# Kernel tuning notes

Hardware: AMD Instinct MI355X
Metric: run time of the kernel (lower is better)

Reference implementation:

```python
import jax, jax.numpy as jnp
import numpy as np

# Canonical topology: root object with K arrays, each array has L number leaves.
# Weights are tied across paths (tie_weights_containers=tie_weights_primitives=True),
# NumberEmbedder runs in eval mode with initial buffers mean=0, sqmean=1 -> identity norm.

K, L, D = 8192, 128, 64


def setup_inputs() -> dict:
    key = jax.random.key(0)
    ks = jax.random.split(key, 16)
    s = 1.0 / np.sqrt(D)
    return {
        "x": jax.random.normal(ks[0], (K, L), dtype=jnp.float32),
        "W_num": jax.random.normal(ks[1], (D, 1), dtype=jnp.float32) * s,
        "b_num": jax.random.normal(ks[2], (D,), dtype=jnp.float32) * s,
        "W_ih": jax.random.normal(ks[3], (4 * D, 2 * D), dtype=jnp.float32) * s,
        "W_hh": jax.random.normal(ks[4], (4 * D, D), dtype=jnp.float32) * s,
        "b_ih": jax.random.normal(ks[5], (4 * D,), dtype=jnp.float32) * s,
        "b_hh": jax.random.normal(ks[6], (4 * D,), dtype=jnp.float32) * s,
        "W_aout": jax.random.normal(ks[7], (D, D), dtype=jnp.float32) * s,
        "b_aout": jax.random.normal(ks[8], (D,), dtype=jnp.float32) * s,
        "W_fh": jax.random.normal(ks[9], (D, D), dtype=jnp.float32) * s,
        "b_fh": jax.random.normal(ks[10], (D,), dtype=jnp.float32) * s,
        "W_iouh": jax.random.normal(ks[11], (3 * D, D), dtype=jnp.float32) * s,
        "b_iouh": jax.random.normal(ks[12], (3 * D,), dtype=jnp.float32) * s,
        "W_oout": jax.random.normal(ks[13], (D, D), dtype=jnp.float32) * s,
        "b_oout": jax.random.normal(ks[14], (D,), dtype=jnp.float32) * s,
    }


def _forward(x, W_num, b_num, W_ih, W_hh, b_ih, b_hh, W_aout, b_aout,
             W_fh, b_fh, W_iouh, b_iouh, W_oout, b_oout):
    d = W_hh.shape[1]
    # --- NumberEmbedder: Linear(1, d) on identity-normalized numbers; c = 0 ---
    emb = x[..., None] * W_num[:, 0] + b_num          # [K, L, d]
    xs = jnp.transpose(emb, (1, 0, 2))                # [L, K, d] time-major for scan
    # --- ArrayEmbedder: LSTMCell over children; input = cat(child_h, child_c) ---
    # child_c is identically zero, so only the first half of W_ih contributes.
    W_ih_h = W_ih[:, :d]                              # [4d, d]
    bias = b_ih + b_hh                                # [4d]

    def step(carry, x_t):
        h, c = carry
        gates = x_t @ W_ih_h.T + h @ W_hh.T + bias    # [K, 4d]
        i, f, g, o = jnp.split(gates, 4, axis=1)
        c2 = jax.nn.sigmoid(f) * c + jax.nn.sigmoid(i) * jnp.tanh(g)
        h2 = jax.nn.sigmoid(o) * jnp.tanh(c2)
        return (h2, c2), None

    h0 = jnp.zeros((x.shape[0], d), dtype=x.dtype)
    (h_arr, c_arr), _ = jax.lax.scan(step, (h0, h0), xs)
    h_hat = h_arr @ W_aout.T + b_aout                 # [K, d] array lout
    # --- ObjectEmbedder: child-sum TreeLSTM over the K array states ---
    f = h_hat @ W_fh.T + b_fh                         # [K, d]
    fc_sum = jnp.sum(jax.nn.sigmoid(f) * c_arr, axis=0, keepdims=True)  # [1, d]
    hs_bar = jnp.sum(h_hat, axis=0, keepdims=True)    # [1, d]
    iou = hs_bar @ W_iouh.T + b_iouh                  # [1, 3d]
    i, o, u = jnp.split(iou, 3, axis=1)
    c_obj = jax.nn.sigmoid(i) * jnp.tanh(u) + fc_sum
    h_obj = jax.nn.sigmoid(o) * jnp.tanh(c_obj)
    h_hat_obj = h_obj @ W_oout.T + b_oout             # [1, d] object lout
    # root forward returns cat(h, c)
    return jnp.concatenate([h_hat_obj, c_obj], axis=1)  # [1, 2d]


def reference(x, W_num, b_num, W_ih, W_hh, b_ih, b_hh, W_aout, b_aout,
              W_fh, b_fh, W_iouh, b_iouh, W_oout, b_oout):
    return _forward(x, W_num, b_num, W_ih, W_hh, b_ih, b_hh, W_aout, b_aout,
                    W_fh, b_fh, W_iouh, b_iouh, W_oout, b_oout)
```

## Files before the change

### kernel.cpp

```cpp
#include <hip/hip_runtime.h>
#include <cstddef>

#define D   64
#define L   128
#define NT  256
#define ROWS 16
#define XSS 132
#define HBS 72
#define NBLK 512
#define LOG2E 1.4426950408889634f

typedef __attribute__((ext_vector_type(8))) short short8;
typedef __attribute__((ext_vector_type(4))) float floatx4;

__device__ __forceinline__ float fast_rcp(float x) {
#if defined(__has_builtin)
#if __has_builtin(__builtin_amdgcn_rcpf)
  return __builtin_amdgcn_rcpf(x);
#else
  return 1.0f / x;
#endif
#else
  return 1.0f / x;
#endif
}
__device__ __forceinline__ float ex2(float x) {
#if defined(__has_builtin)
#if __has_builtin(__builtin_amdgcn_exp2f)
  return __builtin_amdgcn_exp2f(x);
#else
  return __builtin_exp2f(x);
#endif
#else
  return __builtin_exp2f(x);
#endif
}
__device__ __forceinline__ float sig_plain(float x) {
  return fast_rcp(1.0f + ex2(-LOG2E * x));
}
__device__ __forceinline__ float tanh2(float G) {
  return fmaf(2.0f, fast_rcp(1.0f + ex2(G)), -1.0f);
}
__device__ __forceinline__ unsigned short f2bf_rtne(float f) {
  unsigned int u = __float_as_uint(f);
  u += 0x7fffu + ((u >> 16) & 1u);
  return (unsigned short)(u >> 16);
}
__device__ __forceinline__ float bf2f(unsigned short s) {
  return __uint_as_float(((unsigned int)s) << 16);
}
__device__ __forceinline__ void pack_split(float h2, short* hi, short* lo) {
  unsigned int u = __float_as_uint(h2);
  *hi = (short)(u >> 16);
  float hif = __uint_as_float(u & 0xffff0000u);
  *lo = (short)((unsigned short)(__float_as_uint(h2 - hif) >> 16));
}

__global__ __launch_bounds__(NT, 2)
void lstm_main(const float* __restrict__ x,
               const float* __restrict__ W_num,
               const float* __restrict__ b_num,
               const float* __restrict__ W_ih,
               const float* __restrict__ W_hh,
               const float* __restrict__ b_ih,
               const float* __restrict__ b_hh,
               const float* __restrict__ W_aout,
               const float* __restrict__ b_aout,
               const float* __restrict__ W_fh,
               const float* __restrict__ b_fh,
               const float* __restrict__ W_iouh,
               const float* __restrict__ b_iouh,
               const float* __restrict__ W_oout,
               const float* __restrict__ b_oout,
               float* __restrict__ acc_out,
               float* __restrict__ out)
{
  __shared__ __align__(16) float xs[ROWS * XSS];
  __shared__ __align__(16) short hb_hi[2][ROWS * HBS];
  __shared__ __align__(16) short hb_lo[2][ROWS * HBS];
  __shared__ float sacc[2 * D];
  __shared__ float hobj[D];
  __shared__ int   is_last;

  const int tid  = threadIdx.x;
  const int w    = tid >> 6;
  const int lane = tid & 63;
  const int quad = lane >> 4;
  const int c16  = lane & 15;
  const int k0   = blockIdx.x * ROWS;
  const int dcol = w * 16 + c16;

  for (int i = tid; i < ROWS * (L / 4); i += NT) {
    int r = i >> 5, c4 = i & 31;
    float4 v = ((const float4*)(x + (size_t)(k0 + r) * L))[c4];
    float* dst = &xs[r * XSS + c4 * 4];
    dst[0] = v.x; dst[1] = v.y; dst[2] = v.z; dst[3] = v.w;
  }
  for (int i = tid; i < ROWS * HBS; i += NT) { hb_hi[0][i] = 0; hb_lo[0][i] = 0; }

  const float gscale[4] = {-LOG2E, -LOG2E, -2.0f * LOG2E, -LOG2E};

  float An[4], Bc[4];
#pragma unroll
  for (int g = 0; g < 4; ++g) {
    int j = g * 64 + dcol;
    float a = 0.0f, b = b_ih[j] + b_hh[j];
    for (int e = 0; e < D; ++e) {
      float wih = W_ih[(size_t)j * (2 * D) + e];
      a = fmaf(W_num[e], wih, a);
      b = fmaf(b_num[e], wih, b);
    }
    An[g] = a * gscale[g]; Bc[g] = b * gscale[g];
  }

  short8 Bhi[4][2], Blo[4][2];
#pragma unroll
  for (int g = 0; g < 4; ++g) {
#pragma unroll
    for (int kk = 0; kk < 2; ++kk) {
      const float* wp = W_hh + (size_t)(g * 64 + dcol) * D + kk * 32 + quad * 8;
      short8 hi8, lo8;
#pragma unroll
      for (int j = 0; j < 8; ++j) {
        float v = wp[j] * gscale[g];
        unsigned short h = f2bf_rtne(v);
        hi8[j] = (short)h;
        lo8[j] = (short)f2bf_rtne(v - bf2f(h));
      }
      Bhi[g][kk] = hi8; Blo[g][kk] = lo8;
    }
  }

  float creg[4] = {0.f, 0.f, 0.f, 0.f};
  float hreg[4] = {0.f, 0.f, 0.f, 0.f};
  __syncthreads();

  int p = 0;
  for (int t4 = 0; t4 < L; t4 += 4) {
    float4 xq[4];
#pragma unroll
    for (int r = 0; r < 4; ++r)
      xq[r] = *(const float4*)&xs[(quad * 4 + r) * XSS + t4];
#pragma unroll
    for (int u = 0; u < 4; ++u) {
      short8 ahi[2], alo[2];
#pragma unroll
      for (int kk = 0; kk < 2; ++kk) {
        int off = c16 * HBS + kk * 32 + quad * 8;
        ahi[kk] = *(const short8*)&hb_hi[p][off];
        alo[kk] = *(const short8*)&hb_lo[p][off];
      }
      float xv[4] = {xq[0][u], xq[1][u], xq[2][u], xq[3][u]};
      floatx4 acc[4];
#pragma unroll
      for (int g = 0; g < 4; ++g)
        acc[g] = (floatx4){fmaf(An[g], xv[0], Bc[g]), fmaf(An[g], xv[1], Bc[g]),
                           fmaf(An[g], xv[2], Bc[g]), fmaf(An[g], xv[3], Bc[g])};
#pragma unroll
      for (int kk = 0; kk < 2; ++kk) {
#pragma unroll
        for (int g = 0; g < 4; ++g) {
          acc[g] = __builtin_amdgcn_mfma_f32_16x16x32_bf16(ahi[kk], Bhi[g][kk], acc[g], 0, 0, 0);
          acc[g] = __builtin_amdgcn_mfma_f32_16x16x32_bf16(alo[kk], Bhi[g][kk], acc[g], 0, 0, 0);
          acc[g] = __builtin_amdgcn_mfma_f32_16x16x32_bf16(ahi[kk], Blo[g][kk], acc[g], 0, 0, 0);
        }
      }
#pragma unroll
      for (int r = 0; r < 4; ++r) {
        float Ei = ex2(acc[0][r]);
        float Ef = ex2(acc[1][r]);
        float Eg = ex2(acc[2][r]);
        float Eo = ex2(acc[3][r]);
        float pf = 1.0f + Ef, pi = 1.0f + Ei, pg = 1.0f + Eg;
        float mg = 1.0f - Eg;
        float pig = pi * pg;
        float num = fmaf(creg[r], pig, mg * pf);
        float c2  = num * fast_rcp(pf * pig);
        float Ec  = ex2(-2.0f * LOG2E * c2);
        float po = 1.0f + Eo, pc = 1.0f + Ec, mc = 1.0f - Ec;
        float h2 = mc * fast_rcp(po * pc);
        creg[r] = c2;
        hreg[r] = h2;
        short hi, lo;
        pack_split(h2, &hi, &lo);
        int row = quad * 4 + r;
        hb_hi[p ^ 1][row * HBS + dcol] = hi;
        hb_lo[p ^ 1][row * HBS + dcol] = lo;
      }
      __syncthreads();
      p ^= 1;
    }
  }

#pragma unroll
  for (int r = 0; r < 4; ++r) xs[(quad * 4 + r) * XSS + dcol] = hreg[r];
  __syncthreads();

  float hhat[4];
#pragma unroll
  for (int r = 0; r < 4; ++r) {
    float a = b_aout[dcol];
    const float4* wa = (const float4*)(W_aout + (size_t)dcol * D);
    const float* hp = &xs[(quad * 4 + r) * XSS];
#pragma unroll
    for (int e4 = 0; e4 < 16; ++e4) {
      float4 wv = wa[e4];
      a = fmaf(wv.x, hp[e4*4+0], a); a = fmaf(wv.y, hp[e4*4+1], a);
      a = fmaf(wv.z, hp[e4*4+2], a); a = fmaf(wv.w, hp[e4*4+3], a);
    }
    hhat[r] = a;
  }
  __syncthreads();
#pragma unroll
  for (int r = 0; r < 4; ++r) xs[(quad * 4 + r) * XSS + 64 + dcol] = hhat[r];
  __syncthreads();

  float pfc = 0.0f, phs = 0.0f;
#pragma unroll
  for (int r = 0; r < 4; ++r) {
    float f = b_fh[dcol];
    const float4* wf = (const float4*)(W_fh + (size_t)dcol * D);
    const float* hp = &xs[(quad * 4 + r) * XSS + 64];
#pragma unroll
    for (int e4 = 0; e4 < 16; ++e4) {
      float4 wv = wf[e4];
      f = fmaf(wv.x, hp[e4*4+0], f); f = fmaf(wv.y, hp[e4*4+1], f);
      f = fmaf(wv.z, hp[e4*4+2], f); f = fmaf(wv.w, hp[e4*4+3], f);
    }
    pfc = fmaf(sig_plain(f), creg[r], pfc);
    phs += hhat[r];
  }
  pfc += __shfl_xor(pfc, 16); pfc += __shfl_xor(pfc, 32);
  phs += __shfl_xor(phs, 16); phs += __shfl_xor(phs, 32);
  if (quad == 0) {
    atomicAdd(acc_out + dcol, pfc);
    atomicAdd(acc_out + D + dcol, phs);
  }

  __threadfence();
  if (tid == 0) {
    unsigned int prev = __hip_atomic_fetch_add((unsigned int*)(acc_out + 2 * D), 1u,
                                               __ATOMIC_ACQ_REL, __HIP_MEMORY_SCOPE_AGENT);
    is_last = (prev == NBLK - 1) ? 1 : 0;
  }
  __syncthreads();
  if (!is_last) return;
  __threadfence();
  if (tid < 2 * D)
    sacc[tid] = __hip_atomic_load(acc_out + tid, __ATOMIC_RELAXED, __HIP_MEMORY_SCOPE_AGENT);
  __syncthreads();
  if (tid < D) {
    const int d = tid;
    float vi = b_iouh[d], vo = b_iouh[D + d], vu = b_iouh[2 * D + d];
    for (int e = 0; e < D; ++e) {
      float hs = sacc[D + e];
      vi = fmaf(W_iouh[(size_t)d * D + e],           hs, vi);
      vo = fmaf(W_iouh[(size_t)(D + d) * D + e],     hs, vo);
      vu = fmaf(W_iouh[(size_t)(2 * D + d) * D + e], hs, vu);
    }
    float c_obj = sig_plain(vi) * tanh2(-2.0f * LOG2E * vu) + sacc[d];
    float h_obj = sig_plain(vo) * tanh2(-2.0f * LOG2E * c_obj);
    hobj[d] = h_obj;
    out[D + d] = c_obj;
  }
  __syncthreads();
  if (tid < D) {
    const int d = tid;
    float hh = b_oout[d];
    for (int e = 0; e < D; ++e) hh = fmaf(W_oout[(size_t)d * D + e], hobj[e], hh);
    out[d] = hh;
  }
}

extern "C" void kernel_launch(void* const* d_in, const int* in_sizes, int n_in,
                              void* d_out, int out_size, void* d_ws, size_t ws_size,
                              hipStream_t stream) {
  const float* x      = (const float*)d_in[0];
  const float* W_num  = (const float*)d_in[1];
  const float* b_num  = (const float*)d_in[2];
  const float* W_ih   = (const float*)d_in[3];
  const float* W_hh   = (const float*)d_in[4];
  const float* b_ih   = (const float*)d_in[5];
  const float* b_hh   = (const float*)d_in[6];
  const float* W_aout = (const float*)d_in[7];
  const float* b_aout = (const float*)d_in[8];
  const float* W_fh   = (const float*)d_in[9];
  const float* b_fh   = (const float*)d_in[10];
  const float* W_iouh = (const float*)d_in[11];
  const float* b_iouh = (const float*)d_in[12];
  const float* W_oout = (const float*)d_in[13];
  const float* b_oout = (const float*)d_in[14];
  float* acc = (float*)d_ws;
  float* out = (float*)d_out;

  hipMemsetAsync(d_ws, 0, (2 * D + 1) * sizeof(float), stream);
  lstm_main<<<NBLK, NT, 0, stream>>>(x, W_num, b_num, W_ih, W_hh, b_ih, b_hh,
                                     W_aout, b_aout, W_fh, b_fh,
                                     W_iouh, b_iouh, W_oout, b_oout, acc, out);
}
```

Before: 238.2 us.

## Drop bf16 lo-split of hidden state and halve waves per block

Stores the recurrent hidden state as a single bf16 value instead of a hi/lo pair, removing one of the three MFMA passes per gate tile. It also reduces the block to two waves, each owning two column tiles, so per-step work is redistributed and fewer waves join each barrier. The intent is to cut matrix-core work and synchronisation in the serial recurrence. The cost is lower accuracy in the recurrence and more elementwise work and register pressure per wave.

```diff
diff --git a/kernel.cpp b/kernel.cpp
--- a/kernel.cpp
+++ b/kernel.cpp
@@ -3,7 +3,7 @@
 
 #define D   64
 #define L   128
-#define NT  256
+#define NT  128
 #define ROWS 16
 #define XSS 132
 #define HBS 72
@@ -49,14 +49,8 @@
 __device__ __forceinline__ float bf2f(unsigned short s) {
   return __uint_as_float(((unsigned int)s) << 16);
 }
-__device__ __forceinline__ void pack_split(float h2, short* hi, short* lo) {
-  unsigned int u = __float_as_uint(h2);
-  *hi = (short)(u >> 16);
-  float hif = __uint_as_float(u & 0xffff0000u);
-  *lo = (short)((unsigned short)(__float_as_uint(h2 - hif) >> 16));
-}
-
-__global__ __launch_bounds__(NT, 2)
+
+__global__ __launch_bounds__(NT, 1)
 void lstm_main(const float* __restrict__ x,
                const float* __restrict__ W_num,
                const float* __restrict__ b_num,
@@ -76,8 +70,7 @@
                float* __restrict__ out)
 {
   __shared__ __align__(16) float xs[ROWS * XSS];
-  __shared__ __align__(16) short hb_hi[2][ROWS * HBS];
-  __shared__ __align__(16) short hb_lo[2][ROWS * HBS];
+  __shared__ __align__(16) short hb[2][ROWS * HBS];
   __shared__ float sacc[2 * D];
   __shared__ float hobj[D];
   __shared__ int   is_last;
@@ -88,7 +81,6 @@
   const int quad = lane >> 4;
   const int c16  = lane & 15;
   const int k0   = blockIdx.x * ROWS;
-  const int dcol = w * 16 + c16;
 
   for (int i = tid; i < ROWS * (L / 4); i += NT) {
     int r = i >> 5, c4 = i & 31;
@@ -96,29 +88,32 @@
     float* dst = &xs[r * XSS + c4 * 4];
     dst[0] = v.x; dst[1] = v.y; dst[2] = v.z; dst[3] = v.w;
   }
-  for (int i = tid; i < ROWS * HBS; i += NT) { hb_hi[0][i] = 0; hb_lo[0][i] = 0; }
+  for (int i = tid; i < ROWS * HBS; i += NT) hb[0][i] = 0;
 
   const float gscale[4] = {-LOG2E, -LOG2E, -2.0f * LOG2E, -LOG2E};
 
-  float An[4], Bc[4];
-#pragma unroll
-  for (int g = 0; g < 4; ++g) {
-    int j = g * 64 + dcol;
+  float An[8], Bc[8];
+#pragma unroll
+  for (int n = 0; n < 8; ++n) {
+    int g = n >> 1, e = n & 1;
+    int j = g * 64 + (2 * w + e) * 16 + c16;
     float a = 0.0f, b = b_ih[j] + b_hh[j];
-    for (int e = 0; e < D; ++e) {
-      float wih = W_ih[(size_t)j * (2 * D) + e];
-      a = fmaf(W_num[e], wih, a);
-      b = fmaf(b_num[e], wih, b);
-    }
-    An[g] = a * gscale[g]; Bc[g] = b * gscale[g];
-  }
-
-  short8 Bhi[4][2], Blo[4][2];
-#pragma unroll
-  for (int g = 0; g < 4; ++g) {
-#pragma unroll
-    for (int kk = 0; kk < 2; ++kk) {
-      const float* wp = W_hh + (size_t)(g * 64 + dcol) * D + kk * 32 + quad * 8;
+    for (int ee = 0; ee < D; ++ee) {
+      float wih = W_ih[(size_t)j * (2 * D) + ee];
+      a = fmaf(W_num[ee], wih, a);
+      b = fmaf(b_num[ee], wih, b);
+    }
+    An[n] = a * gscale[g]; Bc[n] = b * gscale[g];
+  }
+
+  short8 Bhi[2][8], Blo[2][8];
+#pragma unroll
+  for (int kk = 0; kk < 2; ++kk) {
+#pragma unroll
+    for (int n = 0; n < 8; ++n) {
+      int g = n >> 1, e = n & 1;
+      const float* wp = W_hh + (size_t)(g * 64 + (2 * w + e) * 16 + c16) * D
+                        + kk * 32 + quad * 8;
       short8 hi8, lo8;
 #pragma unroll
       for (int j = 0; j < 8; ++j) {
@@ -127,12 +122,12 @@
         hi8[j] = (short)h;
         lo8[j] = (short)f2bf_rtne(v - bf2f(h));
       }
-      Bhi[g][kk] = hi8; Blo[g][kk] = lo8;
-    }
-  }
-
-  float creg[4] = {0.f, 0.f, 0.f, 0.f};
-  float hreg[4] = {0.f, 0.f, 0.f, 0.f};
+      Bhi[kk][n] = hi8; Blo[kk][n] = lo8;
+    }
+  }
+
+  float creg[8] = {0.f,0.f,0.f,0.f,0.f,0.f,0.f,0.f};
+  float hreg[8] = {0.f,0.f,0.f,0.f,0.f,0.f,0.f,0.f};
   __syncthreads();
 
   int p = 0;
@@ -143,49 +138,46 @@
       xq[r] = *(const float4*)&xs[(quad * 4 + r) * XSS + t4];
 #pragma unroll
     for (int u = 0; u < 4; ++u) {
-      short8 ahi[2], alo[2];
+      short8 ahi[2];
+#pragma unroll
+      for (int kk = 0; kk < 2; ++kk)
+        ahi[kk] = *(const short8*)&hb[p][c16 * HBS + kk * 32 + quad * 8];
+      float xv[4] = {xq[0][u], xq[1][u], xq[2][u], xq[3][u]};
+      floatx4 acc[8];
+#pragma unroll
+      for (int n = 0; n < 8; ++n)
+        acc[n] = (floatx4){fmaf(An[n], xv[0], Bc[n]), fmaf(An[n], xv[1], Bc[n]),
+                           fmaf(An[n], xv[2], Bc[n]), fmaf(An[n], xv[3], Bc[n])};
 #pragma unroll
       for (int kk = 0; kk < 2; ++kk) {
-        int off = c16 * HBS + kk * 32 + quad * 8;
-        ahi[kk] = *(const short8*)&hb_hi[p][off];
-        alo[kk] = *(const short8*)&hb_lo[p][off];
-      }
-      float xv[4] = {xq[0][u], xq[1][u], xq[2][u], xq[3][u]};
-      floatx4 acc[4];
-#pragma unroll
-      for (int g = 0; g < 4; ++g)
-        acc[g] = (floatx4){fmaf(An[g], xv[0], Bc[g]), fmaf(An[g], xv[1], Bc[g]),
-                           fmaf(An[g], xv[2], Bc[g]), fmaf(An[g], xv[3], Bc[g])};
-#pragma unroll
-      for (int kk = 0; kk < 2; ++kk) {
-#pragma unroll
-        for (int g = 0; g < 4; ++g) {
-          acc[g] = __builtin_amdgcn_mfma_f32_16x16x32_bf16(ahi[kk], Bhi[g][kk], acc[g], 0, 0, 0);
-          acc[g] = __builtin_amdgcn_mfma_f32_16x16x32_bf16(alo[kk], Bhi[g][kk], acc[g], 0, 0, 0);
-          acc[g] = __builtin_amdgcn_mfma_f32_16x16x32_bf16(ahi[kk], Blo[g][kk], acc[g], 0, 0, 0);
+#pragma unroll
+        for (int n = 0; n < 8; ++n) {
+          acc[n] = __builtin_amdgcn_mfma_f32_16x16x32_bf16(ahi[kk], Bhi[kk][n], acc[n], 0, 0, 0);
+          acc[n] = __builtin_amdgcn_mfma_f32_16x16x32_bf16(ahi[kk], Blo[kk][n], acc[n], 0, 0, 0);
         }
       }
 #pragma unroll
-      for (int r = 0; r < 4; ++r) {
-        float Ei = ex2(acc[0][r]);
-        float Ef = ex2(acc[1][r]);
-        float Eg = ex2(acc[2][r]);
-        float Eo = ex2(acc[3][r]);
-        float pf = 1.0f + Ef, pi = 1.0f + Ei, pg = 1.0f + Eg;
-        float mg = 1.0f - Eg;
-        float pig = pi * pg;
-        float num = fmaf(creg[r], pig, mg * pf);
-        float c2  = num * fast_rcp(pf * pig);
-        float Ec  = ex2(-2.0f * LOG2E * c2);
-        float po = 1.0f + Eo, pc = 1.0f + Ec, mc = 1.0f - Ec;
-        float h2 = mc * fast_rcp(po * pc);
-        creg[r] = c2;
-        hreg[r] = h2;
-        short hi, lo;
-        pack_split(h2, &hi, &lo);
-        int row = quad * 4 + r;
-        hb_hi[p ^ 1][row * HBS + dcol] = hi;
-        hb_lo[p ^ 1][row * HBS + dcol] = lo;
+      for (int e = 0; e < 2; ++e) {
+#pragma unroll
+        for (int r = 0; r < 4; ++r) {
+          float Ei = ex2(acc[0 + e][r]);
+          float Ef = ex2(acc[2 + e][r]);
+          float Eg = ex2(acc[4 + e][r]);
+          float Eo = ex2(acc[6 + e][r]);
+          float pf = 1.0f + Ef, pi = 1.0f + Ei, pg = 1.0f + Eg;
+          float mg = 1.0f - Eg;
+          float pig = pi * pg;
+          float num = fmaf(creg[e * 4 + r], pig, mg * pf);
+          float c2  = num * fast_rcp(pf * pig);
+          float Ec  = ex2(-2.0f * LOG2E * c2);
+          float po = 1.0f + Eo, pc = 1.0f + Ec, mc = 1.0f - Ec;
+          float h2 = mc * fast_rcp(po * pc);
+          creg[e * 4 + r] = c2;
+          hreg[e * 4 + r] = h2;
+          int row = quad * 4 + r;
+          int d = (2 * w + e) * 16 + c16;
+          hb[p ^ 1][row * HBS + d] = (short)f2bf_rtne(h2);
+        }
       }
       __syncthreads();
       p ^= 1;
@@ -193,48 +185,67 @@
   }
 
 #pragma unroll
-  for (int r = 0; r < 4; ++r) xs[(quad * 4 + r) * XSS + dcol] = hreg[r];
-  __syncthreads();
-
-  float hhat[4];
-#pragma unroll
-  for (int r = 0; r < 4; ++r) {
-    float a = b_aout[dcol];
-    const float4* wa = (const float4*)(W_aout + (size_t)dcol * D);
-    const float* hp = &xs[(quad * 4 + r) * XSS];
-#pragma unroll
-    for (int e4 = 0; e4 < 16; ++e4) {
-      float4 wv = wa[e4];
-      a = fmaf(wv.x, hp[e4*4+0], a); a = fmaf(wv.y, hp[e4*4+1], a);
-      a = fmaf(wv.z, hp[e4*4+2], a); a = fmaf(wv.w, hp[e4*4+3], a);
-    }
-    hhat[r] = a;
-  }
-  __syncthreads();
-#pragma unroll
-  for (int r = 0; r < 4; ++r) xs[(quad * 4 + r) * XSS + 64 + dcol] = hhat[r];
-  __syncthreads();
-
-  float pfc = 0.0f, phs = 0.0f;
-#pragma unroll
-  for (int r = 0; r < 4; ++r) {
-    float f = b_fh[dcol];
-    const float4* wf = (const float4*)(W_fh + (size_t)dcol * D);
-    const float* hp = &xs[(quad * 4 + r) * XSS + 64];
-#pragma unroll
-    for (int e4 = 0; e4 < 16; ++e4) {
-      float4 wv = wf[e4];
-      f = fmaf(wv.x, hp[e4*4+0], f); f = fmaf(wv.y, hp[e4*4+1], f);
-      f = fmaf(wv.z, hp[e4*4+2], f); f = fmaf(wv.w, hp[e4*4+3], f);
-    }
-    pfc = fmaf(sig_plain(f), creg[r], pfc);
-    phs += hhat[r];
-  }
-  pfc += __shfl_xor(pfc, 16); pfc += __shfl_xor(pfc, 32);
-  phs += __shfl_xor(phs, 16); phs += __shfl_xor(phs, 32);
-  if (quad == 0) {
-    atomicAdd(acc_out + dcol, pfc);
-    atomicAdd(acc_out + D + dcol, phs);
+  for (int e = 0; e < 2; ++e)
+#pragma unroll
+    for (int r = 0; r < 4; ++r)
+      xs[(quad * 4 + r) * XSS + (2 * w + e) * 16 + c16] = hreg[e * 4 + r];
+  __syncthreads();
+
+  float hhat[8];
+#pragma unroll
+  for (int e = 0; e < 2; ++e) {
+    int d = (2 * w + e) * 16 + c16;
+    const float4* wa = (const float4*)(W_aout + (size_t)d * D);
+#pragma unroll
+    for (int r = 0; r < 4; ++r) {
+      float a = b_aout[d];
+      const float* hp = &xs[(quad * 4 + r) * XSS];
+#pragma unroll
+      for (int e4 = 0; e4 < 16; ++e4) {
+        float4 wv = wa[e4];
+        a = fmaf(wv.x, hp[e4*4+0], a); a = fmaf(wv.y, hp[e4*4+1], a);
+        a = fmaf(wv.z, hp[e4*4+2], a); a = fmaf(wv.w, hp[e4*4+3], a);
+      }
+      hhat[e * 4 + r] = a;
+    }
+  }
+  __syncthreads();
+#pragma unroll
+  for (int e = 0; e < 2; ++e)
+#pragma unroll
+    for (int r = 0; r < 4; ++r)
+      xs[(quad * 4 + r) * XSS + 64 + (2 * w + e) * 16 + c16] = hhat[e * 4 + r];
+  __syncthreads();
+
+  float pfc[2] = {0.f, 0.f}, phs[2] = {0.f, 0.f};
+#pragma unroll
+  for (int e = 0; e < 2; ++e) {
+    int d = (2 * w + e) * 16 + c16;
+    const float4* wf = (const float4*)(W_fh + (size_t)d * D);
+#pragma unroll
+    for (int r = 0; r < 4; ++r) {
+      float f = b_fh[d];
+      const float* hp = &xs[(quad * 4 + r) * XSS + 64];
+#pragma unroll
+      for (int e4 = 0; e4 < 16; ++e4) {
+        float4 wv = wf[e4];
+        f = fmaf(wv.x, hp[e4*4+0], f); f = fmaf(wv.y, hp[e4*4+1], f);
+        f = fmaf(wv.z, hp[e4*4+2], f); f = fmaf(wv.w, hp[e4*4+3], f);
+      }
+      pfc[e] = fmaf(sig_plain(f), creg[e * 4 + r], pfc[e]);
+      phs[e] += hhat[e * 4 + r];
+    }
+  }
+#pragma unroll
+  for (int e = 0; e < 2; ++e) {
+    float a = pfc[e], b = phs[e];
+    a += __shfl_xor(a, 16); a += __shfl_xor(a, 32);
+    b += __shfl_xor(b, 16); b += __shfl_xor(b, 32);
+    if (quad == 0) {
+      int d = (2 * w + e) * 16 + c16;
+      atomicAdd(acc_out + d, a);
+      atomicAdd(acc_out + D + d, b);
+    }
   }
 
   __threadfence();
```

Result: slower. 246.5 us (+3.4%).
